# Kernel optimization log

Measured on AMD Instinct MI355X. Metric: run time of the kernel, lower is better.

The kernel has to match this reference:

```python
import jax, jax.numpy as jnp
import numpy as np

B = 16384   # tokens
K = 2       # top_k
E = 64      # num_experts
H = 512     # hidden_dim
F = 1024    # expert ffn dim


def setup_inputs() -> dict:
    key = jax.random.key(0)
    k1, k2, k3, k4, k5 = jax.random.split(key, 5)
    hidden_states = jax.random.normal(k1, (B, H), dtype=jnp.float32)
    expert_weights = jax.nn.softmax(jax.random.normal(k2, (B, K), dtype=jnp.float32), axis=-1)
    # Balanced routing: exactly B*K/E assignments per expert (random permutation
    # of a tiled pattern). This is a valid routing for the module and lets the
    # reference use a fixed-capacity grouped GEMM with zero token dropping.
    flat_ids = jax.random.permutation(k3, jnp.tile(jnp.arange(E, dtype=jnp.int32), (B * K) // E))
    expert_ids = flat_ids.reshape(B, K)
    W1 = jax.random.normal(k4, (E, H, F), dtype=jnp.float32) * (1.0 / np.sqrt(H))
    W2 = jax.random.normal(k5, (E, F, H), dtype=jnp.float32) * (1.0 / np.sqrt(F))
    return {"hidden_states": hidden_states, "expert_weights": expert_weights,
            "expert_ids": expert_ids, "W1": W1, "W2": W2}


def reference(hidden_states, expert_weights, expert_ids, W1, W2):
    # Faithful to ExpertGrouping.group_dispatch: every (token, slot) assignment
    # is run through its expert, scaled by its routing weight, and index_add'ed
    # back into the per-token output. Since assignments within an expert are
    # order-independent, we sort assignments by expert id and run one grouped
    # batched GEMM (the fused equivalent of the per-group/per-expert loops).
    b, h = hidden_states.shape
    k = expert_ids.shape[1]
    e = W1.shape[0]
    n = b * k
    cap = n // e  # exact per-expert count (balanced routing)

    flat_ids = expert_ids.reshape(-1)            # [N]
    flat_w = expert_weights.reshape(-1)          # [N]
    token_idx = jnp.arange(n, dtype=jnp.int32) // k  # [N] token for each assignment

    order = jnp.argsort(flat_ids)                # stable sort: groups assignments by expert
    tok_sorted = token_idx[order]                # [N]
    w_sorted = flat_w[order]                     # [N]

    # Gather-dispatch: [E, cap, H]
    xg = hidden_states[tok_sorted].reshape(e, cap, h)
    # Grouped expert FFN (batched over experts)
    hid = jax.nn.silu(jnp.einsum('ech,ehf->ecf', xg, W1))
    yg = jnp.einsum('ecf,efh->ech', hid, W2)     # [E, cap, H]

    # Weighted scatter-combine back to tokens
    weighted = yg.reshape(n, h) * w_sorted[:, None]
    out = jnp.zeros((b, h), dtype=hidden_states.dtype).at[tok_sorted].add(weighted)
    return out
```

## Files before the change

kernel.cpp:

```cpp
#include <hip/hip_runtime.h>
#include <hip/hip_bf16.h>

#define B_TOK 16384
#define TOPK 2
#define NEXP 64
#define HID 512
#define FFN 1024
#define NASSIGN (B_TOK * TOPK)
#define CAP (NASSIGN / NEXP)

typedef unsigned short u16;
typedef __bf16 bf16_t;
typedef bf16_t bf16x8 __attribute__((ext_vector_type(8)));
typedef float f32x4 __attribute__((ext_vector_type(4)));

__device__ __forceinline__ u16 f2bf(float f) {
  union { float f; unsigned u; } v; v.f = f;
  unsigned r = v.u + 0x7fffu + ((v.u >> 16) & 1u);
  return (u16)(r >> 16);
}
__device__ __forceinline__ unsigned pkbf(float a, float b) {
  return (unsigned)f2bf(a) | ((unsigned)f2bf(b) << 16);
}
__device__ __forceinline__ float bf2f(unsigned u16v) {
  union { unsigned u; float f; } v; v.u = u16v << 16; return v.f;
}

#define GLOAD_LDS16(g, l)                                                     \
  __builtin_amdgcn_global_load_lds((const __attribute__((address_space(1))) void*)(g), \
                                   (__attribute__((address_space(3))) void*)(l), 16, 0, 0)

__global__ void k_route(const int* __restrict__ ids, int* __restrict__ cnt,
                        int* __restrict__ tok_of, int* __restrict__ slot_pos) {
  int n = blockIdx.x * blockDim.x + threadIdx.x;
  if (n >= NASSIGN) return;
  int e = ids[n];
  int r = atomicAdd(&cnt[e], 1);
  int p = e * CAP + r;
  tok_of[p] = n >> 1;
  slot_pos[n] = p;
}

__global__ void k_gather(const float* __restrict__ hs, const int* __restrict__ tok_of,
                         u16* __restrict__ Xg) {
  int p = blockIdx.x * 4 + (threadIdx.x >> 6);
  int lane = threadIdx.x & 63;
  const float4* src = reinterpret_cast<const float4*>(hs + (size_t)tok_of[p] * HID);
  uint2* dst = reinterpret_cast<uint2*>(Xg + (size_t)p * HID);
#pragma unroll
  for (int i = 0; i < 2; i++) {
    float4 v = src[i * 64 + lane];
    uint2 o;
    o.x = pkbf(v.x, v.y);
    o.y = pkbf(v.z, v.w);
    dst[i * 64 + lane] = o;
  }
}

template <int K, int NN, bool SILU>
__global__ __launch_bounds__(512, 2) void k_gemm(const u16* __restrict__ A,
                                                 const float* __restrict__ Wf,
                                                 u16* __restrict__ Cout) {
  constexpr int MT = CAP / 256;
  constexpr int NT = NN / 256;
  constexpr int NWG = NEXP * MT * NT;
  constexpr int Q = NWG / 8;
  constexpr int KT = K / 64;
  int wg = (blockIdx.x % 8) * Q + blockIdx.x / 8;
  int e = wg / (MT * NT);
  int rm = wg % (MT * NT);
  int mt = rm / NT, nt = rm % NT;

  const u16* Ab = A + ((size_t)e * CAP + (size_t)mt * 256) * K;

  __shared__ __align__(16) char smc[131072];

  int t_ = threadIdx.x;
  int lane = t_ & 63, wv = t_ >> 6;
  int wm = wv >> 2, wn = wv & 3;
  int l15 = lane & 15, lhi = lane >> 4;

  int srow = t_ >> 3;
  int gchunk = (t_ & 7) ^ (srow & 7);
  const u16* gA = Ab + (size_t)srow * K + gchunk * 8;
#define STAGE_HALF_A(tn, j)                                                  \
  do {                                                                       \
    char* d_ = smc + ((tn) & 1) * 32768 + (j) * 16384 + wv * 1024;           \
    const u16* s_ = gA + (size_t)((j) * 128) * K + (tn) * 64;                \
    GLOAD_LDS16(s_, d_);                                                     \
    GLOAD_LDS16(s_ + (size_t)64 * K, d_ + 8192);                             \
  } while (0)

  int kunit = t_ >> 6;
  int nunit = t_ & 63;
  const float* gWb = Wf + (size_t)e * K * NN + (size_t)(kunit * 8) * NN +
                     (size_t)nt * 256 + nunit * 4;
  int wbo[4];
#pragma unroll
  for (int i = 0; i < 4; i++) {
    int n = nunit * 4 + i;
    int S = (n ^ (n >> 3)) & 7;
    wbo[i] = n * 128 + ((kunit ^ S) << 4);
  }

  f32x4 acc[8][4];
#pragma unroll
  for (int i = 0; i < 8; i++)
#pragma unroll
    for (int j = 0; j < 4; j++) {
      f32x4 z = {0.f, 0.f, 0.f, 0.f};
      acc[i][j] = z;
    }
  bf16x8 a[4][2], b[4][2];

  int aof0 = (wm * 128 + l15) * 128 + ((lhi ^ (l15 & 7)) << 4);
  int aof1 = (wm * 128 + l15) * 128 + (((4 + lhi) ^ (l15 & 7)) << 4);
  int boff[4][2];
#pragma unroll
  for (int nf = 0; nf < 4; nf++) {
    int r = wn * 64 + nf * 16 + l15;
    int Sr = (r ^ (r >> 3)) & 7;
    boff[nf][0] = r * 128 + ((lhi ^ Sr) << 4);
    boff[nf][1] = r * 128 + (((4 + lhi) ^ Sr) << 4);
  }

#define LGKM0_BAR()                                                          \
  do {                                                                       \
    asm volatile("s_waitcnt lgkmcnt(0)" ::: "memory");                       \
    __builtin_amdgcn_sched_barrier(0);                                       \
    __builtin_amdgcn_s_barrier();                                            \
  } while (0)

#define MFMA_QUAD(mh, nh)                                                    \
  do {                                                                       \
    __builtin_amdgcn_s_setprio(1);                                           \
    _Pragma("unroll") for (int mf = 0; mf < 4; mf++)                         \
        _Pragma("unroll") for (int nf = 0; nf < 2; nf++)                     \
            _Pragma("unroll") for (int kk = 0; kk < 2; kk++)                 \
                acc[(mh)*4 + mf][(nh)*2 + nf] = __builtin_amdgcn_mfma_f32_16x16x32_bf16( \
                    a[mf][kk], b[(nh)*2 + nf][kk], acc[(mh)*4 + mf][(nh)*2 + nf], 0, 0, 0); \
    __builtin_amdgcn_s_setprio(0);                                           \
  } while (0)

  STAGE_HALF_A(0, 0); STAGE_HALF_A(0, 1);
  if (KT > 1) { STAGE_HALF_A(1, 0); STAGE_HALF_A(1, 1); }
  {
    float4 P[8];
#pragma unroll
    for (int j = 0; j < 8; j++)
      P[j] = *reinterpret_cast<const float4*>(gWb + (size_t)j * NN);
    char* wB = smc + 65536;
#pragma unroll
    for (int i = 0; i < 4; i++) {
      uint4 v;
      v.x = pkbf(P[0][i], P[1][i]); v.y = pkbf(P[2][i], P[3][i]);
      v.z = pkbf(P[4][i], P[5][i]); v.w = pkbf(P[6][i], P[7][i]);
      *reinterpret_cast<uint4*>(wB + wbo[i]) = v;
    }
  }
  asm volatile("s_waitcnt vmcnt(0)" ::: "memory");
  LGKM0_BAR();

  for (int t = 0; t < KT; t++) {
    const char* pA = smc + (t & 1) * 32768;
    const char* pB = smc + 65536 + (t & 1) * 32768;
    char* wB = smc + 65536 + ((t + 1) & 1) * 32768;
    float4 L0, L1, L2, L3, L4, L5, L6, L7;

#pragma unroll
    for (int mf = 0; mf < 4; mf++) {
      a[mf][0] = *reinterpret_cast<const bf16x8*>(pA + aof0 + mf * 2048);
      a[mf][1] = *reinterpret_cast<const bf16x8*>(pA + aof1 + mf * 2048);
    }
#pragma unroll
    for (int nf = 0; nf < 2; nf++) {
      b[nf][0] = *reinterpret_cast<const bf16x8*>(pB + boff[nf][0]);
      b[nf][1] = *reinterpret_cast<const bf16x8*>(pB + boff[nf][1]);
    }
    if (t + 1 < KT) {
      const float* g = gWb + (size_t)(t + 1) * 64 * NN;
      L0 = *reinterpret_cast<const float4*>(g);
      L1 = *reinterpret_cast<const float4*>(g + (size_t)1 * NN);
      L2 = *reinterpret_cast<const float4*>(g + (size_t)2 * NN);
      L3 = *reinterpret_cast<const float4*>(g + (size_t)3 * NN);
    }
    LGKM0_BAR();
    MFMA_QUAD(0, 0);
    __builtin_amdgcn_s_barrier();

#pragma unroll
    for (int nf = 0; nf < 2; nf++) {
      b[2 + nf][0] = *reinterpret_cast<const bf16x8*>(pB + boff[2 + nf][0]);
      b[2 + nf][1] = *reinterpret_cast<const bf16x8*>(pB + boff[2 + nf][1]);
    }
    if (t + 1 < KT) {
      const float* g = gWb + (size_t)(t + 1) * 64 * NN;
      L4 = *reinterpret_cast<const float4*>(g + (size_t)4 * NN);
      L5 = *reinterpret_cast<const float4*>(g + (size_t)5 * NN);
      L6 = *reinterpret_cast<const float4*>(g + (size_t)6 * NN);
      L7 = *reinterpret_cast<const float4*>(g + (size_t)7 * NN);
    }
    LGKM0_BAR();
    MFMA_QUAD(0, 1);
    __builtin_amdgcn_s_barrier();

#pragma unroll
    for (int mf = 0; mf < 4; mf++) {
      a[mf][0] = *reinterpret_cast<const bf16x8*>(pA + aof0 + (4 + mf) * 2048);
      a[mf][1] = *reinterpret_cast<const bf16x8*>(pA + aof1 + (4 + mf) * 2048);
    }
    LGKM0_BAR();
    MFMA_QUAD(1, 0);
    __builtin_amdgcn_s_barrier();

    if (t + 2 < KT) { STAGE_HALF_A(t + 2, 0); STAGE_HALF_A(t + 2, 1); }
    if (t + 1 < KT) {
      if (t + 2 < KT)
        asm volatile("s_waitcnt vmcnt(4)" ::: "memory");
      else
        asm volatile("s_waitcnt vmcnt(0)" ::: "memory");
      __builtin_amdgcn_sched_barrier(0);
#pragma unroll
      for (int i = 0; i < 4; i++) {
        uint4 v;
        v.x = pkbf(L0[i], L1[i]); v.y = pkbf(L2[i], L3[i]);
        v.z = pkbf(L4[i], L5[i]); v.w = pkbf(L6[i], L7[i]);
        *reinterpret_cast<uint4*>(wB + wbo[i]) = v;
      }
    }
    LGKM0_BAR();
    MFMA_QUAD(1, 1);
    __builtin_amdgcn_s_barrier();
  }
#undef STAGE_HALF_A
#undef MFMA_QUAD
#undef LGKM0_BAR

#pragma unroll
  for (int mf = 0; mf < 8; mf++) {
#pragma unroll
    for (int nf = 0; nf < 4; nf++) {
#pragma unroll
      for (int rg = 0; rg < 4; rg++) {
        float v = acc[mf][nf][rg];
        int grow = mt * 256 + wm * 128 + mf * 16 + lhi * 4 + rg;
        int gcol = nt * 256 + wn * 64 + nf * 16 + l15;
        size_t off = ((size_t)e * CAP + grow) * NN + gcol;
        if constexpr (SILU) v = v / (1.0f + __expf(-v));
        Cout[off] = f2bf(v);
      }
    }
  }
}

__global__ void k_combine(const u16* __restrict__ yws, const int* __restrict__ slot_pos,
                          const float* __restrict__ w, float* __restrict__ out) {
  int tk = blockIdx.x;
  int t = threadIdx.x;
  int p0 = slot_pos[2 * tk], p1 = slot_pos[2 * tk + 1];
  float w0 = w[2 * tk], w1 = w[2 * tk + 1];
  unsigned ua = reinterpret_cast<const unsigned*>(yws + (size_t)p0 * HID)[t];
  unsigned ub = reinterpret_cast<const unsigned*>(yws + (size_t)p1 * HID)[t];
  float2 o;
  o.x = w0 * bf2f(ua & 0xffffu) + w1 * bf2f(ub & 0xffffu);
  o.y = w0 * bf2f(ua >> 16) + w1 * bf2f(ub >> 16);
  reinterpret_cast<float2*>(out + (size_t)tk * HID)[t] = o;
}

extern "C" void kernel_launch(void* const* d_in, const int* in_sizes, int n_in,
                              void* d_out, int out_size, void* d_ws, size_t ws_size,
                              hipStream_t stream) {
  const float* hs = (const float*)d_in[0];
  const float* wts = (const float*)d_in[1];
  const int* ids = (const int*)d_in[2];
  const float* W1 = (const float*)d_in[3];
  const float* W2 = (const float*)d_in[4];
  float* out = (float*)d_out;

  char* ws = (char*)d_ws;
  size_t o = 0;
  int* cnt = (int*)(ws + o);       o += 1024;
  int* slot_pos = (int*)(ws + o);  o += (size_t)NASSIGN * 4;
  int* tok_of = (int*)(ws + o);    o += (size_t)NASSIGN * 4;
  o = (o + 255) & ~(size_t)255;
  u16* Xg = (u16*)(ws + o);        o += (size_t)NASSIGN * HID * 2;
  u16* hid = (u16*)(ws + o);       o += (size_t)NASSIGN * FFN * 2;
  u16* yws = (u16*)(ws + o);       o += (size_t)NASSIGN * HID * 2;

  hipMemsetAsync(cnt, 0, NEXP * sizeof(int), stream);
  k_route<<<(NASSIGN + 255) / 256, 256, 0, stream>>>(ids, cnt, tok_of, slot_pos);
  k_gather<<<NASSIGN / 4, 256, 0, stream>>>(hs, tok_of, Xg);
  k_gemm<HID, FFN, true><<<NEXP * (CAP / 256) * (FFN / 256), 512, 0, stream>>>(Xg, W1, hid);
  k_gemm<FFN, HID, false><<<NEXP * (CAP / 256) * (HID / 256), 512, 0, stream>>>(hid, W2, yws);
  k_combine<<<B_TOK, 256, 0, stream>>>(yws, slot_pos, wts, out);
}
```

Measured before the change: 224.1 us.

## Restructure GEMM pipeline barriers, spread A staging, and stage epilogue through LDS

Reworks the grouped-GEMM main loop. The W prefetch for the next tile is issued all at once at the top, A-tile staging for the next step is spread across the MFMA phases, and the per-phase barrier placement changes so there is one wait per phase. The epilogue now writes SiLU'd accumulators to per-wave LDS scratch and reads them back as rows, giving coalesced 16-byte bf16 stores instead of scattered 2-byte stores. bf16 conversion now uses the native cast. This aims to reduce stalls and store inefficiency, at the cost of higher register pressure from the eight live prefetch float4s and some extra LDS traffic in the epilogue.

```diff
diff --git a/kernel.cpp b/kernel.cpp
--- a/kernel.cpp
+++ b/kernel.cpp
@@ -14,13 +14,13 @@
 typedef bf16_t bf16x8 __attribute__((ext_vector_type(8)));
 typedef float f32x4 __attribute__((ext_vector_type(4)));
 
+__device__ __forceinline__ unsigned pkbf(float a, float b) {
+  union { bf16_t h[2]; unsigned u; } v;
+  v.h[0] = (bf16_t)a; v.h[1] = (bf16_t)b;
+  return v.u;
+}
 __device__ __forceinline__ u16 f2bf(float f) {
-  union { float f; unsigned u; } v; v.f = f;
-  unsigned r = v.u + 0x7fffu + ((v.u >> 16) & 1u);
-  return (u16)(r >> 16);
-}
-__device__ __forceinline__ unsigned pkbf(float a, float b) {
-  return (unsigned)f2bf(a) | ((unsigned)f2bf(b) << 16);
+  union { bf16_t h; u16 u; } v; v.h = (bf16_t)f; return v.u;
 }
 __device__ __forceinline__ float bf2f(unsigned u16v) {
   union { unsigned u; float f; } v; v.u = u16v << 16; return v.f;
@@ -100,7 +100,7 @@
   for (int i = 0; i < 4; i++) {
     int n = nunit * 4 + i;
     int S = (n ^ (n >> 3)) & 7;
-    wbo[i] = n * 128 + ((kunit ^ S) << 4);
+    wbo[i] = 65536 + n * 128 + ((kunit ^ S) << 4);
   }
 
   f32x4 acc[8][4];
@@ -124,11 +124,39 @@
     boff[nf][1] = r * 128 + (((4 + lhi) ^ Sr) << 4);
   }
 
-#define LGKM0_BAR()                                                          \
+#define LOAD_L(tn)                                                           \
+  do {                                                                       \
+    const float* g_ = gWb + (size_t)(tn) * 64 * NN;                          \
+    L0 = *reinterpret_cast<const float4*>(g_);                               \
+    L1 = *reinterpret_cast<const float4*>(g_ + (size_t)1 * NN);              \
+    L2 = *reinterpret_cast<const float4*>(g_ + (size_t)2 * NN);              \
+    L3 = *reinterpret_cast<const float4*>(g_ + (size_t)3 * NN);              \
+    L4 = *reinterpret_cast<const float4*>(g_ + (size_t)4 * NN);              \
+    L5 = *reinterpret_cast<const float4*>(g_ + (size_t)5 * NN);              \
+    L6 = *reinterpret_cast<const float4*>(g_ + (size_t)6 * NN);              \
+    L7 = *reinterpret_cast<const float4*>(g_ + (size_t)7 * NN);              \
+  } while (0)
+
+#define WRITE_B(tn)                                                          \
+  do {                                                                       \
+    char* w_ = smc + ((tn) & 1) * 32768;                                     \
+    _Pragma("unroll") for (int i = 0; i < 4; i++) {                          \
+      uint4 v;                                                               \
+      v.x = pkbf(L0[i], L1[i]); v.y = pkbf(L2[i], L3[i]);                    \
+      v.z = pkbf(L4[i], L5[i]); v.w = pkbf(L6[i], L7[i]);                    \
+      *reinterpret_cast<uint4*>(w_ + wbo[i]) = v;                            \
+    }                                                                        \
+  } while (0)
+
+#define SBAR()                                                               \
+  do {                                                                       \
+    __builtin_amdgcn_sched_barrier(0);                                       \
+    __builtin_amdgcn_s_barrier();                                            \
+  } while (0)
+#define LGKM0()                                                              \
   do {                                                                       \
     asm volatile("s_waitcnt lgkmcnt(0)" ::: "memory");                       \
     __builtin_amdgcn_sched_barrier(0);                                       \
-    __builtin_amdgcn_s_barrier();                                            \
   } while (0)
 
 #define MFMA_QUAD(mh, nh)                                                    \
@@ -142,31 +170,22 @@
     __builtin_amdgcn_s_setprio(0);                                           \
   } while (0)
 
+  float4 L0, L1, L2, L3, L4, L5, L6, L7;
+
   STAGE_HALF_A(0, 0); STAGE_HALF_A(0, 1);
-  if (KT > 1) { STAGE_HALF_A(1, 0); STAGE_HALF_A(1, 1); }
-  {
-    float4 P[8];
-#pragma unroll
-    for (int j = 0; j < 8; j++)
-      P[j] = *reinterpret_cast<const float4*>(gWb + (size_t)j * NN);
-    char* wB = smc + 65536;
-#pragma unroll
-    for (int i = 0; i < 4; i++) {
-      uint4 v;
-      v.x = pkbf(P[0][i], P[1][i]); v.y = pkbf(P[2][i], P[3][i]);
-      v.z = pkbf(P[4][i], P[5][i]); v.w = pkbf(P[6][i], P[7][i]);
-      *reinterpret_cast<uint4*>(wB + wbo[i]) = v;
-    }
-  }
+  LOAD_L(0);
   asm volatile("s_waitcnt vmcnt(0)" ::: "memory");
-  LGKM0_BAR();
-
+  __builtin_amdgcn_sched_barrier(0);
+  WRITE_B(0);
+  LGKM0();
+  __builtin_amdgcn_s_barrier();
+
+#pragma unroll 2
   for (int t = 0; t < KT; t++) {
     const char* pA = smc + (t & 1) * 32768;
     const char* pB = smc + 65536 + (t & 1) * 32768;
-    char* wB = smc + 65536 + ((t + 1) & 1) * 32768;
-    float4 L0, L1, L2, L3, L4, L5, L6, L7;
-
+
+    if (t + 1 < KT) LOAD_L(t + 1);
 #pragma unroll
     for (int mf = 0; mf < 4; mf++) {
       a[mf][0] = *reinterpret_cast<const bf16x8*>(pA + aof0 + mf * 2048);
@@ -177,80 +196,75 @@
       b[nf][0] = *reinterpret_cast<const bf16x8*>(pB + boff[nf][0]);
       b[nf][1] = *reinterpret_cast<const bf16x8*>(pB + boff[nf][1]);
     }
-    if (t + 1 < KT) {
-      const float* g = gWb + (size_t)(t + 1) * 64 * NN;
-      L0 = *reinterpret_cast<const float4*>(g);
-      L1 = *reinterpret_cast<const float4*>(g + (size_t)1 * NN);
-      L2 = *reinterpret_cast<const float4*>(g + (size_t)2 * NN);
-      L3 = *reinterpret_cast<const float4*>(g + (size_t)3 * NN);
-    }
-    LGKM0_BAR();
+    SBAR(); LGKM0();
     MFMA_QUAD(0, 0);
-    __builtin_amdgcn_s_barrier();
-
+
+    if (t + 1 < KT) STAGE_HALF_A(t + 1, 0);
 #pragma unroll
     for (int nf = 0; nf < 2; nf++) {
       b[2 + nf][0] = *reinterpret_cast<const bf16x8*>(pB + boff[2 + nf][0]);
       b[2 + nf][1] = *reinterpret_cast<const bf16x8*>(pB + boff[2 + nf][1]);
     }
-    if (t + 1 < KT) {
-      const float* g = gWb + (size_t)(t + 1) * 64 * NN;
-      L4 = *reinterpret_cast<const float4*>(g + (size_t)4 * NN);
-      L5 = *reinterpret_cast<const float4*>(g + (size_t)5 * NN);
-      L6 = *reinterpret_cast<const float4*>(g + (size_t)6 * NN);
-      L7 = *reinterpret_cast<const float4*>(g + (size_t)7 * NN);
-    }
-    LGKM0_BAR();
+    SBAR(); LGKM0();
     MFMA_QUAD(0, 1);
-    __builtin_amdgcn_s_barrier();
-
+
+    if (t + 1 < KT) STAGE_HALF_A(t + 1, 1);
 #pragma unroll
     for (int mf = 0; mf < 4; mf++) {
       a[mf][0] = *reinterpret_cast<const bf16x8*>(pA + aof0 + (4 + mf) * 2048);
       a[mf][1] = *reinterpret_cast<const bf16x8*>(pA + aof1 + (4 + mf) * 2048);
     }
-    LGKM0_BAR();
+    SBAR(); LGKM0();
     MFMA_QUAD(1, 0);
-    __builtin_amdgcn_s_barrier();
-
-    if (t + 2 < KT) { STAGE_HALF_A(t + 2, 0); STAGE_HALF_A(t + 2, 1); }
+
     if (t + 1 < KT) {
-      if (t + 2 < KT)
-        asm volatile("s_waitcnt vmcnt(4)" ::: "memory");
-      else
-        asm volatile("s_waitcnt vmcnt(0)" ::: "memory");
+      asm volatile("s_waitcnt vmcnt(4)" ::: "memory");
       __builtin_amdgcn_sched_barrier(0);
-#pragma unroll
-      for (int i = 0; i < 4; i++) {
-        uint4 v;
-        v.x = pkbf(L0[i], L1[i]); v.y = pkbf(L2[i], L3[i]);
-        v.z = pkbf(L4[i], L5[i]); v.w = pkbf(L6[i], L7[i]);
-        *reinterpret_cast<uint4*>(wB + wbo[i]) = v;
-      }
-    }
-    LGKM0_BAR();
+      WRITE_B(t + 1);
+    }
+    SBAR(); LGKM0();
     MFMA_QUAD(1, 1);
-    __builtin_amdgcn_s_barrier();
+    asm volatile("s_waitcnt vmcnt(0)" ::: "memory");
+    SBAR();
   }
 #undef STAGE_HALF_A
+#undef LOAD_L
+#undef WRITE_B
 #undef MFMA_QUAD
-#undef LGKM0_BAR
-
-#pragma unroll
-  for (int mf = 0; mf < 8; mf++) {
-#pragma unroll
-    for (int nf = 0; nf < 4; nf++) {
-#pragma unroll
-      for (int rg = 0; rg < 4; rg++) {
-        float v = acc[mf][nf][rg];
-        int grow = mt * 256 + wm * 128 + mf * 16 + lhi * 4 + rg;
-        int gcol = nt * 256 + wn * 64 + nf * 16 + l15;
-        size_t off = ((size_t)e * CAP + grow) * NN + gcol;
-        if constexpr (SILU) v = v / (1.0f + __expf(-v));
-        Cout[off] = f2bf(v);
-      }
-    }
-  }
+
+  {
+    char* reg_ = smc + wv * 4352;
+    u16* Cb = Cout + ((size_t)e * CAP + mt * 256 + wm * 128) * NN +
+              (size_t)nt * 256 + wn * 64;
+    int rr = lane >> 2;
+    int cg = (lane & 3) * 16;
+    for (int mf = 0; mf < 8; mf++) {
+#pragma unroll
+      for (int nf = 0; nf < 4; nf++)
+#pragma unroll
+        for (int rg = 0; rg < 4; rg++) {
+          float v = acc[mf][nf][rg];
+          if constexpr (SILU) v = v / (1.0f + __expf(-v));
+          *reinterpret_cast<float*>(reg_ + (lhi * 4 + rg) * 272 + (nf * 16 + l15) * 4) = v;
+        }
+      LGKM0();
+      f32x4 q0 = *reinterpret_cast<const f32x4*>(reg_ + rr * 272 + cg * 4);
+      f32x4 q1 = *reinterpret_cast<const f32x4*>(reg_ + rr * 272 + cg * 4 + 16);
+      f32x4 q2 = *reinterpret_cast<const f32x4*>(reg_ + rr * 272 + cg * 4 + 32);
+      f32x4 q3 = *reinterpret_cast<const f32x4*>(reg_ + rr * 272 + cg * 4 + 48);
+      LGKM0();
+      uint4 s0, s1;
+      s0.x = pkbf(q0[0], q0[1]); s0.y = pkbf(q0[2], q0[3]);
+      s0.z = pkbf(q1[0], q1[1]); s0.w = pkbf(q1[2], q1[3]);
+      s1.x = pkbf(q2[0], q2[1]); s1.y = pkbf(q2[2], q2[3]);
+      s1.z = pkbf(q3[0], q3[1]); s1.w = pkbf(q3[2], q3[3]);
+      u16* row = Cb + (size_t)(mf * 16 + rr) * NN + cg;
+      *reinterpret_cast<uint4*>(row) = s0;
+      *reinterpret_cast<uint4*>(row + 8) = s1;
+    }
+  }
+#undef SBAR
+#undef LGKM0
 }
 
 __global__ void k_combine(const u16* __restrict__ yws, const int* __restrict__ slot_pos,
```

New measurement: 348.3 us. 55.4% more time.
